# Optimization experiments

Measured on AMD Instinct MI355X. Metric: run time of the kernel, lower is better.

## Reference

```python
import jax, jax.numpy as jnp
import numpy as np

N_NODES = 100000

def _graphconv_both(x, Wr, edges):
    # DGL GraphConv, norm='both', bias=False, allow_zero_in_degree=True:
    # out = D_in^{-1/2} * A^T_scatter( D_out^{-1/2}[src] * (X @ W)[src] )
    src, dst = edges[0], edges[1]
    ones = jnp.ones(src.shape[0], dtype=x.dtype)
    out_deg = jnp.clip(jax.ops.segment_sum(ones, src, num_segments=N_NODES), 1.0)
    in_deg = jnp.clip(jax.ops.segment_sum(ones, dst, num_segments=N_NODES), 1.0)
    norm_src = jax.lax.rsqrt(out_deg)  # [N]
    norm_dst = jax.lax.rsqrt(in_deg)   # [N]
    h = x @ Wr                          # [N, out] (mult W first since in>out)
    msg = h[src] * norm_src[src][:, None]          # [E, out]
    agg = jax.ops.segment_sum(msg, dst, num_segments=N_NODES)  # [N, out]
    return agg * norm_dst[:, None]


def setup_inputs() -> dict:
    key = jax.random.key(0)
    k1, k2, k3, k4 = jax.random.split(key, 4)
    x = jax.random.normal(k1, (N_NODES, 256), dtype=jnp.float32)
    W = jax.random.normal(k2, (4, 256, 64), dtype=jnp.float32) * 0.05
    src = jax.random.randint(k3, (4, 1, 1600000), 0, N_NODES)
    dst = jax.random.randint(k4, (4, 1, 1600000), 0, N_NODES)
    edge_index = jnp.concatenate([src, dst], axis=1).astype(jnp.int64)  # [4,2,E]
    return {"x": x, "W": W, "edge_index": edge_index}


def reference(x, W, edge_index):
    # per-relation GraphConv, stacked & summed, then tanh; dropout rate 0 -> identity
    per_rel = jax.vmap(lambda Wr, e: _graphconv_both(x, Wr, e))(W, edge_index)  # [R,N,out]
    Z = per_rel.sum(0)
    return jnp.tanh(Z)
```

## Files before the change

### kernel.cpp

```cpp
#include <hip/hip_runtime.h>
#include <hip/hip_bf16.h>

#define NN 100000
#define EPR 1600000
#define FIN 256
#define FOUT 64
#define BSZ 64
#define NB 1563
#define NBP 1568
#define CHUNK 4096
#define NBLK 391
#define EPT 16
#define CAP 4096

typedef __attribute__((ext_vector_type(8))) short short8;
typedef __attribute__((ext_vector_type(4))) float f32x4;

__device__ __forceinline__ unsigned short f2bf(float f) {
    unsigned u = __float_as_uint(f);
    u = (u + 0x7FFFu + ((u >> 16) & 1u)) >> 16;
    return (unsigned short)u;
}
__device__ __forceinline__ float bf2f(unsigned short v) {
    return __uint_as_float(((unsigned)v) << 16);
}

__global__ __launch_bounds__(256) void hist_all_kernel(const int* __restrict__ ei,
                                                       unsigned* __restrict__ btabD4,
                                                       unsigned* __restrict__ btabS4) {
    __shared__ unsigned hD[NB], hS[NB];
    int tid = threadIdx.x, r = blockIdx.y, blk = blockIdx.x;
    const int* src = ei + (size_t)r * 2 * EPR;
    const int* dst = src + EPR;
    for (int i = tid; i < NB; i += 256) { hD[i] = 0; hS[i] = 0; }
    __syncthreads();
    int e0 = blk * CHUNK;
    #pragma unroll
    for (int t = 0; t < EPT; ++t) {
        int e = e0 + t * 256 + tid;
        if (e < EPR) {
            atomicAdd(&hS[src[e] >> 6], 1u);
            atomicAdd(&hD[dst[e] >> 6], 1u);
        }
    }
    __syncthreads();
    size_t row = ((size_t)r * NBLK + blk) * NBP;
    for (int i = tid; i < NB; i += 256) {
        btabD4[row + i] = hD[i];
        btabS4[row + i] = hS[i];
    }
}

__global__ __launch_bounds__(256) void btot_all_kernel(unsigned* __restrict__ btabD4,
                                                       unsigned* __restrict__ btabS4,
                                                       unsigned* __restrict__ totD4,
                                                       unsigned* __restrict__ totS4) {
    int r = blockIdx.z;
    unsigned* tab = (blockIdx.y ? btabS4 : btabD4) + (size_t)r * NBLK * NBP;
    unsigned* tot = (blockIdx.y ? totS4 : totD4) + (size_t)r * NBP;
    __shared__ unsigned tile[NBLK][8];
    int b0 = blockIdx.x * 8;
    for (int idx = threadIdx.x; idx < NBLK * 8; idx += 256) {
        int blk = idx >> 3, bb = idx & 7;
        int b = b0 + bb;
        tile[blk][bb] = (b < NB) ? tab[(size_t)blk * NBP + b] : 0u;
    }
    __syncthreads();
    if (threadIdx.x < 8) {
        int bb = threadIdx.x;
        unsigned s = 0;
        for (int blk = 0; blk < NBLK; ++blk) {
            unsigned v = tile[blk][bb];
            tile[blk][bb] = s;
            s += v;
        }
        if (b0 + bb < NB) tot[b0 + bb] = s;
    }
    __syncthreads();
    for (int idx = threadIdx.x; idx < NBLK * 8; idx += 256) {
        int blk = idx >> 3, bb = idx & 7;
        int b = b0 + bb;
        if (b < NB) tab[(size_t)blk * NBP + b] = tile[blk][bb];
    }
}

__global__ void scan_all_kernel(const unsigned* __restrict__ totD4, const unsigned* __restrict__ totS4,
                                unsigned* __restrict__ gbaseD4, unsigned* __restrict__ gbaseS4) {
    int r = blockIdx.y;
    const unsigned* tot = (blockIdx.x ? totS4 : totD4) + (size_t)r * NBP;
    unsigned* gb = (blockIdx.x ? gbaseS4 : gbaseD4) + (size_t)r * NBP;
    __shared__ unsigned sc[256];
    int tid = threadIdx.x;
    unsigned loc[8]; unsigned s = 0;
    #pragma unroll
    for (int k = 0; k < 8; ++k) {
        int idx = tid * 8 + k;
        unsigned v = (idx < NB) ? tot[idx] : 0u;
        loc[k] = s; s += v;
    }
    sc[tid] = s; __syncthreads();
    for (int off = 1; off < 256; off <<= 1) {
        unsigned a = (tid >= off) ? sc[tid - off] : 0u;
        __syncthreads(); sc[tid] += a; __syncthreads();
    }
    unsigned texcl = tid ? sc[tid - 1] : 0u;
    #pragma unroll
    for (int k = 0; k < 8; ++k) {
        int idx = tid * 8 + k;
        if (idx < NB) gb[idx] = texcl + loc[k];
    }
}

__global__ __launch_bounds__(256) void placeD_all_kernel(const int* __restrict__ ei,
                                                         const unsigned* __restrict__ gbaseD4,
                                                         const unsigned* __restrict__ btabD4,
                                                         unsigned* __restrict__ pairs4) {
    __shared__ unsigned h[NB], hloc[NB], hbase[NB], sc[256];
    __shared__ unsigned buf[CHUNK], buf2[CHUNK];
    int tid = threadIdx.x, blk = blockIdx.x, r = blockIdx.y;
    const int* src = ei + (size_t)r * 2 * EPR;
    const int* dst = src + EPR;
    const unsigned* gbase = gbaseD4 + (size_t)r * NBP;
    const unsigned* pblk = btabD4 + ((size_t)r * NBLK + blk) * NBP;
    unsigned* pairs = pairs4 + (size_t)r * EPR;
    int e0 = blk * CHUNK;
    int csize = EPR - e0; if (csize > CHUNK) csize = CHUNK;

    for (int i = tid; i < NB; i += 256) h[i] = 0;
    __syncthreads();

    int es[EPT], ed[EPT];
    #pragma unroll
    for (int t = 0; t < EPT; ++t) {
        int e = e0 + t * 256 + tid;
        if (e < EPR) { es[t] = src[e]; ed[t] = dst[e]; atomicAdd(&h[ed[t] >> 6], 1u); }
        else { es[t] = -1; ed[t] = 0; }
    }
    __syncthreads();

    unsigned loc[8]; unsigned s = 0;
    #pragma unroll
    for (int k = 0; k < 8; ++k) {
        int idx = tid * 8 + k;
        unsigned v = (idx < NB) ? h[idx] : 0u;
        loc[k] = s; s += v;
    }
    sc[tid] = s; __syncthreads();
    for (int off = 1; off < 256; off <<= 1) {
        unsigned a = (tid >= off) ? sc[tid - off] : 0u;
        __syncthreads(); sc[tid] += a; __syncthreads();
    }
    unsigned texcl = tid ? sc[tid - 1] : 0u;
    #pragma unroll
    for (int k = 0; k < 8; ++k) {
        int idx = tid * 8 + k;
        if (idx < NB) hloc[idx] = texcl + loc[k];
    }
    __syncthreads();

    for (int i = tid; i < NB; i += 256) hbase[i] = gbase[i] + pblk[i];
    __syncthreads();
    for (int i = tid; i < NB; i += 256) h[i] = 0;
    __syncthreads();

    #pragma unroll
    for (int t = 0; t < EPT; ++t) {
        if (es[t] >= 0) {
            int b = ed[t] >> 6;
            unsigned rr = atomicAdd(&h[b], 1u);
            unsigned slot = hloc[b] + rr;
            buf[slot] = (unsigned)es[t] | ((unsigned)(ed[t] & 63) << 17);
            buf2[slot] = hbase[b] + rr;
        }
    }
    __syncthreads();

    for (int k = tid; k < csize; k += 256)
        pairs[buf2[k]] = buf[k];
}

__global__ __launch_bounds__(256) void placeS_all_kernel(const int* __restrict__ ei,
                                                         const unsigned* __restrict__ gbaseS4,
                                                         const unsigned* __restrict__ btabS4,
                                                         unsigned char* __restrict__ pairs2_4) {
    __shared__ unsigned h[NB], hloc[NB], hbase[NB], sc[256];
    __shared__ unsigned char bufB[CHUNK];
    __shared__ unsigned buf2[CHUNK];
    int tid = threadIdx.x, blk = blockIdx.x, r = blockIdx.y;
    const int* src = ei + (size_t)r * 2 * EPR;
    const unsigned* gbase = gbaseS4 + (size_t)r * NBP;
    const unsigned* pblk = btabS4 + ((size_t)r * NBLK + blk) * NBP;
    unsigned char* pairs2 = pairs2_4 + (size_t)r * EPR;
    int e0 = blk * CHUNK;
    int csize = EPR - e0; if (csize > CHUNK) csize = CHUNK;

    for (int i = tid; i < NB; i += 256) h[i] = 0;
    __syncthreads();

    int es[EPT];
    #pragma unroll
    for (int t = 0; t < EPT; ++t) {
        int e = e0 + t * 256 + tid;
        if (e < EPR) { es[t] = src[e]; atomicAdd(&h[es[t] >> 6], 1u); }
        else es[t] = -1;
    }
    __syncthreads();

    unsigned loc[8]; unsigned s = 0;
    #pragma unroll
    for (int k = 0; k < 8; ++k) {
        int idx = tid * 8 + k;
        unsigned v = (idx < NB) ? h[idx] : 0u;
        loc[k] = s; s += v;
    }
    sc[tid] = s; __syncthreads();
    for (int off = 1; off < 256; off <<= 1) {
        unsigned a = (tid >= off) ? sc[tid - off] : 0u;
        __syncthreads(); sc[tid] += a; __syncthreads();
    }
    unsigned texcl = tid ? sc[tid - 1] : 0u;
    #pragma unroll
    for (int k = 0; k < 8; ++k) {
        int idx = tid * 8 + k;
        if (idx < NB) hloc[idx] = texcl + loc[k];
    }
    __syncthreads();

    for (int i = tid; i < NB; i += 256) hbase[i] = gbase[i] + pblk[i];
    __syncthreads();
    for (int i = tid; i < NB; i += 256) h[i] = 0;
    __syncthreads();

    #pragma unroll
    for (int t = 0; t < EPT; ++t) {
        if (es[t] >= 0) {
            int b = es[t] >> 6;
            unsigned rr = atomicAdd(&h[b], 1u);
            unsigned slot = hloc[b] + rr;
            bufB[slot] = (unsigned char)(es[t] & 63);
            buf2[slot] = hbase[b] + rr;
        }
    }
    __syncthreads();

    for (int k = tid; k < csize; k += 256)
        pairs2[buf2[k]] = bufB[k];
}

__global__ void srcdeg_all_kernel(const unsigned char* __restrict__ pairs2_4,
                                  const unsigned* __restrict__ gbaseS4,
                                  const unsigned* __restrict__ totS4,
                                  float* __restrict__ nsb4) {
    __shared__ unsigned cnt[BSZ];
    int tid = threadIdx.x, b = blockIdx.x, r = blockIdx.y;
    const unsigned char* pairs2 = pairs2_4 + (size_t)r * EPR;
    if (tid < BSZ) cnt[tid] = 0;
    __syncthreads();
    unsigned st = gbaseS4[(size_t)r * NBP + b];
    int n = (int)totS4[(size_t)r * NBP + b];
    for (int i = tid; i < n; i += 256)
        atomicAdd(&cnt[pairs2[st + i]], 1u);
    __syncthreads();
    if (tid < BSZ) {
        int node = b * BSZ + tid;
        if (node < NN) {
            unsigned c = cnt[tid]; if (c < 1u) c = 1u;
            nsb4[(size_t)r * NN + node] = rsqrtf((float)c);
        }
    }
}

__global__ __launch_bounds__(256, 2) void gemm4_kernel(const float* __restrict__ x,
                                                       const float* __restrict__ W,
                                                       unsigned short* __restrict__ hsb4,
                                                       const float* __restrict__ nsb4) {
    __shared__ unsigned short xs[128][40];
    __shared__ unsigned short wt[4][64][40];
    int tid = threadIdx.x;
    int wave = tid >> 6, lane = tid & 63;
    int wm = (wave >> 1) * 64;
    int wn = (wave & 1) * 32;
    int m0 = blockIdx.x * 128;

    f32x4 acc[4][4][2];
    #pragma unroll
    for (int r = 0; r < 4; ++r)
        #pragma unroll
        for (int mi = 0; mi < 4; ++mi)
            #pragma unroll
            for (int ni = 0; ni < 2; ++ni)
                acc[r][mi][ni] = (f32x4){0.f, 0.f, 0.f, 0.f};

    int srow = tid >> 1, skp = (tid & 1) * 16;
    int swn = tid >> 2, skq = (tid & 3) * 8;
    int gr = m0 + srow; if (gr >= NN) gr = NN - 1;
    const float* xrow = &x[(size_t)gr * FIN];

    for (int k0 = 0; k0 < FIN; k0 += 32) {
        #pragma unroll
        for (int q = 0; q < 4; ++q) {
            float4 v = *(const float4*)(xrow + k0 + skp + q * 4);
            unsigned lo = (unsigned)f2bf(v.x) | ((unsigned)f2bf(v.y) << 16);
            unsigned hi = (unsigned)f2bf(v.z) | ((unsigned)f2bf(v.w) << 16);
            *(uint2*)&xs[srow][skp + q * 4] = make_uint2(lo, hi);
        }
        #pragma unroll
        for (int r = 0; r < 4; ++r) {
            const float* w = W + (size_t)r * FIN * FOUT;
            unsigned pk[4];
            #pragma unroll
            for (int i = 0; i < 8; i += 2) {
                unsigned short b0 = f2bf(w[(size_t)(k0 + skq + i) * FOUT + swn]);
                unsigned short b1 = f2bf(w[(size_t)(k0 + skq + i + 1) * FOUT + swn]);
                pk[i >> 1] = (unsigned)b0 | ((unsigned)b1 << 16);
            }
            *(uint4*)&wt[r][swn][skq] = make_uint4(pk[0], pk[1], pk[2], pk[3]);
        }
        __syncthreads();

        int fr = lane & 15, fk = (lane >> 4) * 8;
        short8 af[4];
        #pragma unroll
        for (int mi = 0; mi < 4; ++mi) af[mi] = *(const short8*)&xs[wm + mi * 16 + fr][fk];
        #pragma unroll
        for (int r = 0; r < 4; ++r) {
            short8 b0 = *(const short8*)&wt[r][wn + fr][fk];
            short8 b1 = *(const short8*)&wt[r][wn + 16 + fr][fk];
            #pragma unroll
            for (int mi = 0; mi < 4; ++mi) {
                acc[r][mi][0] = __builtin_amdgcn_mfma_f32_16x16x32_bf16(af[mi], b0, acc[r][mi][0], 0, 0, 0);
                acc[r][mi][1] = __builtin_amdgcn_mfma_f32_16x16x32_bf16(af[mi], b1, acc[r][mi][1], 0, 0, 0);
            }
        }
        __syncthreads();
    }

    int fr = lane & 15, frow4 = (lane >> 4) * 4;
    #pragma unroll
    for (int r = 0; r < 4; ++r) {
        unsigned short* hsb = hsb4 + (size_t)r * NN * FOUT;
        const float* ns = nsb4 + (size_t)r * NN;
        #pragma unroll
        for (int mi = 0; mi < 4; ++mi) {
            #pragma unroll
            for (int rg = 0; rg < 4; ++rg) {
                int grow = m0 + wm + mi * 16 + frow4 + rg;
                if (grow < NN) {
                    float sc2 = ns[grow];
                    #pragma unroll
                    for (int ni = 0; ni < 2; ++ni) {
                        int gcol = wn + ni * 16 + fr;
                        hsb[(size_t)grow * FOUT + gcol] = f2bf(acc[r][mi][ni][rg] * sc2);
                    }
                }
            }
        }
    }
}

__global__ __launch_bounds__(512, 8) void aggsort4_kernel(const unsigned* __restrict__ pairs4,
                                                          const unsigned* __restrict__ gbaseD4,
                                                          const unsigned* __restrict__ totD4,
                                                          const unsigned short* __restrict__ hsb4,
                                                          float* __restrict__ out) {
    __shared__ unsigned sorted[CAP];
    __shared__ unsigned cnt[BSZ];
    __shared__ unsigned loff[BSZ + 1];
    int tid = threadIdx.x;
    int b = blockIdx.x;
    int wave = tid >> 6, lane = tid & 63;

    float acc[8];
    #pragma unroll
    for (int i = 0; i < 8; ++i) acc[i] = 0.f;

    for (int r = 0; r < 4; ++r) {
        const unsigned* pairs = pairs4 + (size_t)r * EPR;
        const unsigned short* hsb = hsb4 + (size_t)r * NN * FOUT;
        unsigned start = gbaseD4[(size_t)r * NBP + b];
        int n = (int)totD4[(size_t)r * NBP + b];

        __syncthreads();
        if (tid < BSZ) cnt[tid] = 0;
        __syncthreads();

        if (n <= CAP) {
            unsigned rec[CAP / 512];
            #pragma unroll
            for (int t = 0; t < CAP / 512; ++t) {
                int i = t * 512 + tid;
                rec[t] = 0xFFFFFFFFu;
                if (i < n) {
                    rec[t] = pairs[start + i];
                    atomicAdd(&cnt[rec[t] >> 17], 1u);
                }
            }
            __syncthreads();
            if (wave == 0) {
                unsigned v = cnt[lane];
                unsigned sum = v;
                #pragma unroll
                for (int o = 1; o < 64; o <<= 1) {
                    unsigned u = __shfl_up(sum, o);
                    if (lane >= o) sum += u;
                }
                loff[lane + 1] = sum;
                if (lane == 0) loff[0] = 0;
                cnt[lane] = sum - v;
            }
            __syncthreads();
            #pragma unroll
            for (int t = 0; t < CAP / 512; ++t) {
                if (rec[t] != 0xFFFFFFFFu) {
                    unsigned p = atomicAdd(&cnt[rec[t] >> 17], 1u);
                    sorted[p] = rec[t];
                }
            }
            __syncthreads();

            for (int i = 0; i < 8; ++i) {
                int nl = wave * 8 + i;
                int node = b * BSZ + nl;
                if (node >= NN) break;
                int lo = (int)loff[nl], hi = (int)loff[nl + 1];
                float seg = 0.f;
                for (int j0 = lo; j0 < hi; j0 += 8) {
                    #pragma unroll
                    for (int u = 0; u < 8; ++u) {
                        int j = j0 + u;
                        unsigned q = sorted[(j < hi) ? j : lo];
                        float v = bf2f(hsb[(size_t)(q & 0x1FFFF) * FOUT + lane]);
                        seg += (j < hi) ? v : 0.f;
                    }
                }
                int deg = hi - lo; if (deg < 1) deg = 1;
                acc[i] += seg * rsqrtf((float)deg);
            }
        } else {
            for (int i = 0; i < 8; ++i) {
                int nl = wave * 8 + i;
                int node = b * BSZ + nl;
                if (node >= NN) break;
                float seg = 0.f; int deg = 0;
                for (int base2 = 0; base2 < n; base2 += 64) {
                    int m = n - base2; if (m > 64) m = 64;
                    unsigned sl = (base2 + lane < n) ? pairs[start + base2 + lane] : 0xFFFFFFFFu;
                    for (int j = 0; j < m; ++j) {
                        unsigned q = __shfl(sl, j);
                        if ((int)(q >> 17) == nl) {
                            seg += bf2f(hsb[(size_t)(q & 0x1FFFF) * FOUT + lane]);
                            ++deg;
                        }
                    }
                }
                if (deg < 1) deg = 1;
                acc[i] += seg * rsqrtf((float)deg);
            }
        }
    }

    #pragma unroll
    for (int i = 0; i < 8; ++i) {
        int nl = wave * 8 + i;
        int node = b * BSZ + nl;
        if (node < NN)
            out[(size_t)node * FOUT + lane] = tanhf(acc[i]);
    }
}

extern "C" void kernel_launch(void* const* d_in, const int* in_sizes, int n_in,
                              void* d_out, int out_size, void* d_ws, size_t ws_size,
                              hipStream_t stream) {
    const float* x = (const float*)d_in[0];
    const float* W = (const float*)d_in[1];
    const int* ei = (const int*)d_in[2];
    float* out = (float*)d_out;

    char* ws = (char*)d_ws;
    size_t o = 0;
    unsigned short* hsb4 = (unsigned short*)(ws + o); o += (size_t)4 * NN * FOUT * 2;
    unsigned* pairs4 = (unsigned*)(ws + o);   o += (size_t)4 * EPR * 4;
    unsigned char* pairs2_4 = (unsigned char*)(ws + o); o += (size_t)4 * EPR;
    unsigned* btabD4 = (unsigned*)(ws + o);   o += (size_t)4 * NBLK * NBP * 4;
    unsigned* btabS4 = (unsigned*)(ws + o);   o += (size_t)4 * NBLK * NBP * 4;
    unsigned* totD4 = (unsigned*)(ws + o);    o += (size_t)4 * NBP * 4;
    unsigned* totS4 = (unsigned*)(ws + o);    o += (size_t)4 * NBP * 4;
    unsigned* gbaseD4 = (unsigned*)(ws + o);  o += (size_t)4 * NBP * 4;
    unsigned* gbaseS4 = (unsigned*)(ws + o);  o += (size_t)4 * NBP * 4;
    float* nsb4 = (float*)(ws + o);           o += (size_t)4 * NN * 4;

    hist_all_kernel<<<dim3(NBLK, 4), 256, 0, stream>>>(ei, btabD4, btabS4);
    btot_all_kernel<<<dim3((NB + 7) / 8, 2, 4), 256, 0, stream>>>(btabD4, btabS4, totD4, totS4);
    scan_all_kernel<<<dim3(2, 4), 256, 0, stream>>>(totD4, totS4, gbaseD4, gbaseS4);
    placeD_all_kernel<<<dim3(NBLK, 4), 256, 0, stream>>>(ei, gbaseD4, btabD4, pairs4);
    placeS_all_kernel<<<dim3(NBLK, 4), 256, 0, stream>>>(ei, gbaseS4, btabS4, pairs2_4);
    srcdeg_all_kernel<<<dim3(NB, 4), 256, 0, stream>>>(pairs2_4, gbaseS4, totS4, nsb4);
    gemm4_kernel<<<(NN + 127) / 128, 256, 0, stream>>>(x, W, hsb4, nsb4);
    aggsort4_kernel<<<NB, 512, 0, stream>>>(pairs4, gbaseD4, totD4, hsb4, out);
}
```

Baseline: 415.4 us.

## Vectorize gather: 16 lanes per row loading 4 bf16, 4 edges per wave step

The aggregation kernel now has each wave process four edges at once. Each 16-lane group loads 8 bytes (4 bf16 features) of one source row instead of one bf16 per lane. Per-node segments are padded to multiples of 4 and filled with a dummy zero row appended to each relation's feature table, which avoids bounds checks. Partial sums are combined with cross-lane shuffles and written as float4. The change adds a dummy row, a padding fill pass and extra shared memory, and lowers the occupancy hint from 8 to 4. The fallback path for oversized buckets is rewritten to scan pairs serially.

New measurement: 526.8 us. 26.8% more time.

```diff
diff --git a/kernel.cpp b/kernel.cpp
--- a/kernel.cpp
+++ b/kernel.cpp
@@ -12,6 +12,7 @@
 #define NBLK 391
 #define EPT 16
 #define CAP 4096
+#define HSTRIDE ((size_t)(NN + 1) * FOUT)
 
 typedef __attribute__((ext_vector_type(8))) short short8;
 typedef __attribute__((ext_vector_type(4))) float f32x4;
@@ -24,6 +25,7 @@
 __device__ __forceinline__ float bf2f(unsigned short v) {
     return __uint_as_float(((unsigned)v) << 16);
 }
+__device__ __forceinline__ float uaf(unsigned u) { return __uint_as_float(u); }
 
 __global__ __launch_bounds__(256) void hist_all_kernel(const int* __restrict__ ei,
                                                        unsigned* __restrict__ btabD4,
@@ -338,7 +340,7 @@
     int fr = lane & 15, frow4 = (lane >> 4) * 4;
     #pragma unroll
     for (int r = 0; r < 4; ++r) {
-        unsigned short* hsb = hsb4 + (size_t)r * NN * FOUT;
+        unsigned short* hsb = hsb4 + (size_t)r * HSTRIDE;
         const float* ns = nsb4 + (size_t)r * NN;
         #pragma unroll
         for (int mi = 0; mi < 4; ++mi) {
@@ -356,27 +358,36 @@
             }
         }
     }
-}
-
-__global__ __launch_bounds__(512, 8) void aggsort4_kernel(const unsigned* __restrict__ pairs4,
+    if (blockIdx.x == 0 && tid < FOUT) {
+        #pragma unroll
+        for (int r = 0; r < 4; ++r)
+            hsb4[(size_t)r * HSTRIDE + (size_t)NN * FOUT + tid] = 0;
+    }
+}
+
+__global__ __launch_bounds__(512, 4) void aggsort4_kernel(const unsigned* __restrict__ pairs4,
                                                           const unsigned* __restrict__ gbaseD4,
                                                           const unsigned* __restrict__ totD4,
                                                           const unsigned short* __restrict__ hsb4,
                                                           float* __restrict__ out) {
-    __shared__ unsigned sorted[CAP];
+    __shared__ unsigned sorted[CAP + 256];
     __shared__ unsigned cnt[BSZ];
+    __shared__ unsigned tdeg[BSZ];
     __shared__ unsigned loff[BSZ + 1];
     int tid = threadIdx.x;
     int b = blockIdx.x;
     int wave = tid >> 6, lane = tid & 63;
-
-    float acc[8];
-    #pragma unroll
-    for (int i = 0; i < 8; ++i) acc[i] = 0.f;
+    int lg = lane >> 4;
+    int lp = lane & 15;
+    const unsigned DUMMY = (unsigned)NN;
+
+    f32x4 acc4[8];
+    #pragma unroll
+    for (int i = 0; i < 8; ++i) acc4[i] = (f32x4){0.f, 0.f, 0.f, 0.f};
 
     for (int r = 0; r < 4; ++r) {
         const unsigned* pairs = pairs4 + (size_t)r * EPR;
-        const unsigned short* hsb = hsb4 + (size_t)r * NN * FOUT;
+        const char* hsbB = (const char*)(hsb4 + (size_t)r * HSTRIDE);
         unsigned start = gbaseD4[(size_t)r * NBP + b];
         int n = (int)totD4[(size_t)r * NBP + b];
 
@@ -384,7 +395,7 @@
         if (tid < BSZ) cnt[tid] = 0;
         __syncthreads();
 
-        if (n <= CAP) {
+        if (n <= CAP - 192) {
             unsigned rec[CAP / 512];
             #pragma unroll
             for (int t = 0; t < CAP / 512; ++t) {
@@ -398,7 +409,8 @@
             __syncthreads();
             if (wave == 0) {
                 unsigned v = cnt[lane];
-                unsigned sum = v;
+                unsigned pad = (v + 3u) & ~3u;
+                unsigned sum = pad;
                 #pragma unroll
                 for (int o = 1; o < 64; o <<= 1) {
                     unsigned u = __shfl_up(sum, o);
@@ -406,8 +418,12 @@
                 }
                 loff[lane + 1] = sum;
                 if (lane == 0) loff[0] = 0;
-                cnt[lane] = sum - v;
-            }
+                tdeg[lane] = v;
+                cnt[lane] = sum - pad;
+            }
+            __syncthreads();
+            int ptot = (int)loff[BSZ];
+            for (int i = tid; i < ptot; i += 512) sorted[i] = DUMMY;
             __syncthreads();
             #pragma unroll
             for (int t = 0; t < CAP / 512; ++t) {
@@ -418,43 +434,56 @@
             }
             __syncthreads();
 
+            #pragma unroll
             for (int i = 0; i < 8; ++i) {
                 int nl = wave * 8 + i;
                 int node = b * BSZ + nl;
                 if (node >= NN) break;
                 int lo = (int)loff[nl], hi = (int)loff[nl + 1];
-                float seg = 0.f;
-                for (int j0 = lo; j0 < hi; j0 += 8) {
-                    #pragma unroll
-                    for (int u = 0; u < 8; ++u) {
-                        int j = j0 + u;
-                        unsigned q = sorted[(j < hi) ? j : lo];
-                        float v = bf2f(hsb[(size_t)(q & 0x1FFFF) * FOUT + lane]);
-                        seg += (j < hi) ? v : 0.f;
-                    }
+                f32x4 seg = (f32x4){0.f, 0.f, 0.f, 0.f};
+                for (int j0 = lo; j0 < hi; j0 += 4) {
+                    unsigned q = sorted[j0 + lg];
+                    uint2 u = *(const uint2*)(hsbB + (((size_t)(q & 0x1FFFF)) << 7) + (lp << 3));
+                    seg.x += uaf(u.x << 16);
+                    seg.y += uaf(u.x & 0xFFFF0000u);
+                    seg.z += uaf(u.y << 16);
+                    seg.w += uaf(u.y & 0xFFFF0000u);
                 }
-                int deg = hi - lo; if (deg < 1) deg = 1;
-                acc[i] += seg * rsqrtf((float)deg);
+                unsigned d = tdeg[nl]; if (d < 1u) d = 1u;
+                float ndv = rsqrtf((float)d);
+                acc4[i].x += seg.x * ndv;
+                acc4[i].y += seg.y * ndv;
+                acc4[i].z += seg.z * ndv;
+                acc4[i].w += seg.w * ndv;
             }
         } else {
             for (int i = 0; i < 8; ++i) {
                 int nl = wave * 8 + i;
                 int node = b * BSZ + nl;
                 if (node >= NN) break;
-                float seg = 0.f; int deg = 0;
-                for (int base2 = 0; base2 < n; base2 += 64) {
-                    int m = n - base2; if (m > 64) m = 64;
-                    unsigned sl = (base2 + lane < n) ? pairs[start + base2 + lane] : 0xFFFFFFFFu;
-                    for (int j = 0; j < m; ++j) {
-                        unsigned q = __shfl(sl, j);
-                        if ((int)(q >> 17) == nl) {
-                            seg += bf2f(hsb[(size_t)(q & 0x1FFFF) * FOUT + lane]);
+                f32x4 seg = (f32x4){0.f, 0.f, 0.f, 0.f};
+                int deg = 0;
+                for (int j = 0; j < n; ++j) {
+                    unsigned q = pairs[start + j];
+                    if ((int)(q >> 17) == nl) {
+                        uint2 u = *(const uint2*)(hsbB + (((size_t)(q & 0x1FFFF)) << 7) + (lp << 3));
+                        if (lg == 0) {
                             ++deg;
                         }
+                        seg.x += uaf(u.x << 16);
+                        seg.y += uaf(u.x & 0xFFFF0000u);
+                        seg.z += uaf(u.y << 16);
+                        seg.w += uaf(u.y & 0xFFFF0000u);
                     }
                 }
+                deg = 0;
+                for (int j = 0; j < n; ++j) deg += ((int)(pairs[start + j] >> 17) == nl);
                 if (deg < 1) deg = 1;
-                acc[i] += seg * rsqrtf((float)deg);
+                float ndv = rsqrtf((float)deg) * 0.25f;
+                acc4[i].x += seg.x * ndv;
+                acc4[i].y += seg.y * ndv;
+                acc4[i].z += seg.z * ndv;
+                acc4[i].w += seg.w * ndv;
             }
         }
     }
@@ -463,8 +492,16 @@
     for (int i = 0; i < 8; ++i) {
         int nl = wave * 8 + i;
         int node = b * BSZ + nl;
-        if (node < NN)
-            out[(size_t)node * FOUT + lane] = tanhf(acc[i]);
+        f32x4 v = acc4[i];
+        v.x += __shfl_xor(v.x, 16); v.y += __shfl_xor(v.y, 16);
+        v.z += __shfl_xor(v.z, 16); v.w += __shfl_xor(v.w, 16);
+        v.x += __shfl_xor(v.x, 32); v.y += __shfl_xor(v.y, 32);
+        v.z += __shfl_xor(v.z, 32); v.w += __shfl_xor(v.w, 32);
+        if (node < NN && lg == 0) {
+            float4 o;
+            o.x = tanhf(v.x); o.y = tanhf(v.y); o.z = tanhf(v.z); o.w = tanhf(v.w);
+            *(float4*)&out[(size_t)node * FOUT + lp * 4] = o;
+        }
     }
 }
 
@@ -478,7 +515,7 @@
 
     char* ws = (char*)d_ws;
     size_t o = 0;
-    unsigned short* hsb4 = (unsigned short*)(ws + o); o += (size_t)4 * NN * FOUT * 2;
+    unsigned short* hsb4 = (unsigned short*)(ws + o); o += (size_t)4 * HSTRIDE * 2;
     unsigned* pairs4 = (unsigned*)(ws + o);   o += (size_t)4 * EPR * 4;
     unsigned char* pairs2_4 = (unsigned char*)(ws + o); o += (size_t)4 * EPR;
     unsigned* btabD4 = (unsigned*)(ws + o);   o += (size_t)4 * NBLK * NBP * 4;
```
